# Performance work log

Measured on AMD Instinct MI355X. Metric: run time of the kernel, lower is better.

## Reference

```python
import jax, jax.numpy as jnp
import numpy as np

N_BINS = 64
SIGMA_SCALE = 0.5
_LAB_RANGES = {'L': (0.0, 100.0), 'a': (-128.0, 127.0), 'b': (-128.0, 127.0)}


def _channel_params(vmin, vmax, n_bins=N_BINS, sigma_scale=SIGMA_SCALE):
    delta = (vmax - vmin) / n_bins
    centers = jnp.linspace(vmin + delta / 2, vmax - delta / 2, n_bins, dtype=jnp.float32)
    sigma = jnp.float32(delta * sigma_scale)
    return centers, sigma


def rgb_to_lab(rgb):
    # rgb: (B, 3, H, W) in [0, 1] sRGB
    thr = 0.04045
    lin = jnp.where(rgb > thr, jnp.power((rgb + 0.055) / 1.055, 2.4), rgb / 12.92)
    r, g, b = lin[:, 0], lin[:, 1], lin[:, 2]
    # sRGB -> XYZ (D65)
    x = 0.412453 * r + 0.357580 * g + 0.180423 * b
    y = 0.212671 * r + 0.715160 * g + 0.072169 * b
    z = 0.019334 * r + 0.119193 * g + 0.950227 * b
    xn, zn = 0.950456, 1.088754  # D65 white (Y normalized to 1)
    x = x / xn
    z = z / zn
    eps = 0.008856
    def f(t):
        return jnp.where(t > eps, jnp.cbrt(t), 7.787 * t + 16.0 / 116.0)
    fx, fy, fz = f(x), f(y), f(z)
    L = 116.0 * fy - 16.0
    a = 500.0 * (fx - fy)
    bb = 200.0 * (fy - fz)
    return jnp.stack([L, a, bb], axis=1)  # (B, 3, H, W)


def setup_inputs() -> dict:
    key = jax.random.key(0)
    img = jax.random.uniform(key, (16, 3, 512, 512), dtype=jnp.float32)
    return {"img": img}


def reference(img) -> jnp.ndarray:
    B = img.shape[0]
    img_lab = rgb_to_lab(img)  # (B, 3, H, W)
    parts = []
    for c_idx, name in enumerate(['L', 'a', 'b']):
        centers, sigma = _channel_params(*_LAB_RANGES[name])
        pixels = img_lab[:, c_idx].reshape(B, -1)  # (B, HW)
        diff = pixels[:, :, None] - centers[None, None, :]  # (B, HW, n_bins)
        weights = jnp.exp(-(diff ** 2) / (2.0 * sigma ** 2))
        hist_unnorm = weights.sum(axis=1)  # (B, n_bins)
        hist = hist_unnorm / (hist_unnorm.sum(axis=-1, keepdims=True) + 1e-8)
        parts.append(hist)
    return jnp.concatenate(parts, axis=1)  # (B, 192)
```

## Files before the change

### kernel.cpp

```cpp
#include <hip/hip_runtime.h>
#include <cmath>

#define HW (512*512)
#define NSUB 2048
#define THREADS1 1024
#define BLKS_PER_IMG 32

__device__ __forceinline__ float fexp2(float x) { return __builtin_amdgcn_exp2f(x); }
__device__ __forceinline__ float flog2(float x) { return __builtin_amdgcn_logf(x); }

__global__ __launch_bounds__(THREADS1) void count_conv_kernel(const float* __restrict__ img,
                                                              float* __restrict__ part) {
    __shared__ unsigned sh[2][3 * NSUB];
    __shared__ float hb[3][64];
    const int tid = threadIdx.x;
    unsigned* flat = &sh[0][0];
    for (int i = tid; i < 2 * 3 * NSUB; i += THREADS1) flat[i] = 0u;
    __syncthreads();

    unsigned* h = sh[(tid >> 6) & 1];

    const int b  = blockIdx.y;
    const int bx = blockIdx.x;
    const float* base = img + (size_t)b * 3u * HW;

    const int p = (bx * THREADS1 + tid) * 8;
    float4 r4a = *reinterpret_cast<const float4*>(base + p);
    float4 r4b = *reinterpret_cast<const float4*>(base + p + 4);
    float4 g4a = *reinterpret_cast<const float4*>(base + p + HW);
    float4 g4b = *reinterpret_cast<const float4*>(base + p + HW + 4);
    float4 b4a = *reinterpret_cast<const float4*>(base + p + 2 * HW);
    float4 b4b = *reinterpret_cast<const float4*>(base + p + 2 * HW + 4);
    float rr[8] = {r4a.x, r4a.y, r4a.z, r4a.w, r4b.x, r4b.y, r4b.z, r4b.w};
    float gg[8] = {g4a.x, g4a.y, g4a.z, g4a.w, g4b.x, g4b.y, g4b.z, g4b.w};
    float bl[8] = {b4a.x, b4a.y, b4a.z, b4a.w, b4b.x, b4b.y, b4b.z, b4b.w};

    #pragma unroll
    for (int k = 0; k < 8; ++k) {
        float lr = (rr[k] > 0.04045f) ? fexp2(2.4f * flog2((rr[k] + 0.055f) * (1.0f / 1.055f))) : rr[k] * (1.0f / 12.92f);
        float lg = (gg[k] > 0.04045f) ? fexp2(2.4f * flog2((gg[k] + 0.055f) * (1.0f / 1.055f))) : gg[k] * (1.0f / 12.92f);
        float lb = (bl[k] > 0.04045f) ? fexp2(2.4f * flog2((bl[k] + 0.055f) * (1.0f / 1.055f))) : bl[k] * (1.0f / 12.92f);

        float x = 0.4339530f * lr + 0.3762197f * lg + 0.1898288f * lb;
        float y = 0.2126710f * lr + 0.7151600f * lg + 0.0721690f * lb;
        float z = 0.0177578f * lr + 0.1094766f * lg + 0.8727661f * lb;

        float fx = (x > 0.008856f) ? fexp2(flog2(x) * (1.0f/3.0f)) : 7.787f * x + 16.0f/116.0f;
        float fy = (y > 0.008856f) ? fexp2(flog2(y) * (1.0f/3.0f)) : 7.787f * y + 16.0f/116.0f;
        float fz = (z > 0.008856f) ? fexp2(flog2(z) * (1.0f/3.0f)) : 7.787f * z + 16.0f/116.0f;

        int iL = (int)(2375.68f    * fy - 327.68f);
        int iA = (int)(4015.6863f  * (fx - fy) + 1028.01569f);
        int iB = (int)(1606.27451f * (fy - fz) + 1028.01569f);

        atomicAdd(&h[iL], 1u);
        atomicAdd(&h[NSUB + iA], 1u);
        atomicAdd(&h[2 * NSUB + iB], 1u);
    }
    __syncthreads();

    float* subf = reinterpret_cast<float*>(&sh[0][0]);
    for (int i = tid; i < 3 * NSUB; i += THREADS1) {
        unsigned s = sh[0][i] + sh[1][i];
        subf[i] = (float)s;
    }
    __syncthreads();

    const int j = tid >> 4;
    const int q = tid & 15;
    const float C = 2.8853901f;
    const float jf = (float)j + 0.5f - (0.5f / 32.0f);
    const int s_lo = 32 * j - 86;
    #pragma unroll
    for (int ch = 0; ch < 3; ++ch) {
        float acc = 0.0f;
        #pragma unroll
        for (int i = 0; i < 13; ++i) {
            int off = q + 16 * i;
            int s = s_lo + off;
            if (off < 204 && (unsigned)s < (unsigned)NSUB) {
                float d = (float)s * (1.0f / 32.0f) - jf;
                acc += subf[ch * NSUB + s] * fexp2(-C * d * d);
            }
        }
        acc += __shfl_xor(acc, 1, 64);
        acc += __shfl_xor(acc, 2, 64);
        acc += __shfl_xor(acc, 4, 64);
        acc += __shfl_xor(acc, 8, 64);
        if (q == 0) hb[ch][j] = acc;
    }
    __syncthreads();

    if (tid < 192) {
        float* dst = part + (size_t)(b * BLKS_PER_IMG + bx) * 192;
        dst[tid] = (&hb[0][0])[tid];
    }
}

__global__ __launch_bounds__(192) void finalize_kernel(const float* __restrict__ part,
                                                       float* __restrict__ out) {
    const int b = blockIdx.x;
    const int t = threadIdx.x;
    const float* p0 = part + (size_t)b * BLKS_PER_IMG * 192 + t;
    float v = 0.0f;
    #pragma unroll
    for (int k = 0; k < BLKS_PER_IMG; ++k) v += p0[k * 192];
    float s = v;
    #pragma unroll
    for (int off = 32; off >= 1; off >>= 1) s += __shfl_down(s, off, 64);
    s = __shfl(s, 0, 64);
    out[b * 192 + t] = v / (s + 1e-8f);
}

extern "C" void kernel_launch(void* const* d_in, const int* in_sizes, int n_in,
                              void* d_out, int out_size, void* d_ws, size_t ws_size,
                              hipStream_t stream) {
    const float* img = (const float*)d_in[0];
    float* out     = (float*)d_out;
    float* part    = (float*)d_ws;

    const int B = in_sizes[0] / (3 * HW);

    count_conv_kernel<<<dim3(BLKS_PER_IMG, B), THREADS1, 0, stream>>>(img, part);
    finalize_kernel<<<B, 192, 0, stream>>>(part, out);
}
```

Baseline: 89.44 us.

## Interleave LDS histogram copies by lane parity and tabulate Gaussian convolution weights

Result: faster. 87.40 us (-2.3%).

```diff
diff --git a/kernel.cpp b/kernel.cpp
--- a/kernel.cpp
+++ b/kernel.cpp
@@ -5,20 +5,31 @@
 #define NSUB 2048
 #define THREADS1 1024
 #define BLKS_PER_IMG 32
+#define TBL (3 * NSUB + 1)
+#define NTAP 160
 
 __device__ __forceinline__ float fexp2(float x) { return __builtin_amdgcn_exp2f(x); }
 __device__ __forceinline__ float flog2(float x) { return __builtin_amdgcn_logf(x); }
 
 __global__ __launch_bounds__(THREADS1) void count_conv_kernel(const float* __restrict__ img,
                                                               float* __restrict__ part) {
-    __shared__ unsigned sh[2][3 * NSUB];
+    __align__(16) __shared__ unsigned sh[2 * TBL + 2];
+    __shared__ float W[NTAP];
     __shared__ float hb[3][64];
     const int tid = threadIdx.x;
-    unsigned* flat = &sh[0][0];
-    for (int i = tid; i < 2 * 3 * NSUB; i += THREADS1) flat[i] = 0u;
+    {
+        uint4* z = reinterpret_cast<uint4*>(sh);
+        const uint4 zero = {0u, 0u, 0u, 0u};
+        for (int i = tid; i < (2 * TBL + 2) / 4; i += THREADS1) z[i] = zero;
+    }
+    if (tid < NTAP) {
+        const float C = 2.8853901f;
+        float d = ((float)tid - 63.5f) * (1.0f / 32.0f) - 0.5f;
+        W[tid] = fexp2(-C * d * d);
+    }
     __syncthreads();
 
-    unsigned* h = sh[(tid >> 6) & 1];
+    unsigned* h = sh + (tid & 1) * TBL;
 
     const int b  = blockIdx.y;
     const int bx = blockIdx.x;
@@ -59,29 +70,25 @@
     }
     __syncthreads();
 
-    float* subf = reinterpret_cast<float*>(&sh[0][0]);
+    float* subf = reinterpret_cast<float*>(sh);
     for (int i = tid; i < 3 * NSUB; i += THREADS1) {
-        unsigned s = sh[0][i] + sh[1][i];
+        unsigned s = sh[i] + sh[TBL + i];
         subf[i] = (float)s;
     }
     __syncthreads();
 
     const int j = tid >> 4;
     const int q = tid & 15;
-    const float C = 2.8853901f;
-    const float jf = (float)j + 0.5f - (0.5f / 32.0f);
-    const int s_lo = 32 * j - 86;
+    const int s_lo = 32 * j - 64;
     #pragma unroll
     for (int ch = 0; ch < 3; ++ch) {
         float acc = 0.0f;
         #pragma unroll
-        for (int i = 0; i < 13; ++i) {
-            int off = q + 16 * i;
-            int s = s_lo + off;
-            if (off < 204 && (unsigned)s < (unsigned)NSUB) {
-                float d = (float)s * (1.0f / 32.0f) - jf;
-                acc += subf[ch * NSUB + s] * fexp2(-C * d * d);
-            }
+        for (int i = 0; i < 10; ++i) {
+            int t = q + 16 * i;
+            int s = s_lo + t;
+            if ((unsigned)s < (unsigned)NSUB)
+                acc += subf[ch * NSUB + s] * W[t];
         }
         acc += __shfl_xor(acc, 1, 64);
         acc += __shfl_xor(acc, 2, 64);
```
